# Optimization experiments

Hardware: AMD Instinct MI355X
Metric: run time of the kernel (lower is better)

## Reference

```python
import jax, jax.numpy as jnp
import numpy as np

IN_DIM, OUT_DIM, NUM, K = 512, 512, 5, 3
BATCH = 4096


def extend_grid(grid, k):
    # grid: (in_dim, num+1) -> (in_dim, num+1+2k), uniform step extension on both sides
    h = (grid[:, -1:] - grid[:, :1]) / (grid.shape[1] - 1)
    left = grid[:, :1] - h * jnp.arange(k, 0, -1, dtype=grid.dtype)
    right = grid[:, -1:] + h * jnp.arange(1, k + 1, dtype=grid.dtype)
    return jnp.concatenate([left, grid, right], axis=1)


def b_batch(x, grid, k):
    # Cox-de Boor recursion. x: (in_dim, batch), grid: (in_dim, G) extended.
    xe = x[:, None, :]            # (in, 1, B)
    g = grid[:, :, None]          # (in, G, 1)
    B = ((xe >= g[:, :-1]) & (xe < g[:, 1:])).astype(x.dtype)  # degree-0 indicators
    for p in range(1, k + 1):     # unrolled over small fixed k
        left = (xe - g[:, : -(p + 1)]) / (g[:, p:-1] - g[:, : -(p + 1)])
        right = (g[:, p + 1:] - xe) / (g[:, p + 1:] - g[:, 1:-p])
        B = left * B[:, :-1] + right * B[:, 1:]
    return B                      # (in_dim, NUM+K, batch)


def kan_forward(x, grid, weight, bias):
    batch = x.shape[0]
    xt = x.T                                            # (in, B)
    sp = b_batch(xt, extend_grid(grid, K), K)           # (in, num+k, B)
    sp = jnp.transpose(sp, (2, 1, 0))                   # (B, num+k, in)
    sb = jax.nn.silu(x)[:, None, :]                     # (B, 1, in)  base_fun branch
    gs = jnp.concatenate([sp, sb], axis=1)              # (B, num+k+1, in)
    acts = (gs * x[:, None, :]).reshape(batch, -1)      # einsum 'ijk,ik->ijk' + flatten
    return acts @ weight.T + bias                       # (B, out_dim)


def setup_inputs() -> dict:
    key = jax.random.key(0)
    k1, k2, k3 = jax.random.split(key, 3)
    x = jax.random.uniform(k1, (BATCH, IN_DIM), jnp.float32, -1.0, 1.0)
    grid = jnp.tile(jnp.linspace(-1.0, 1.0, NUM + 1, dtype=jnp.float32)[None, :], (IN_DIM, 1))
    in_multi = IN_DIM * (NUM + K + 1)
    weight = jax.random.normal(k2, (OUT_DIM, in_multi), jnp.float32) / np.sqrt(in_multi).astype(np.float32)
    bias = jax.random.normal(k3, (OUT_DIM,), jnp.float32) * 0.01
    return {"x": x, "grid": grid, "weight": weight, "bias": bias}


def reference(x, grid, weight, bias):
    return kan_forward(x, grid, weight, bias)
```

## Files before the change

kernel.cpp:

```cpp
#include <hip/hip_runtime.h>
#include <hip/hip_bf16.h>

#define IN_DIM  512
#define OUT_DIM 512
#define BATCH   4096
#define NBASIS  9
#define KDIM    (IN_DIM * NBASIS)

#define WOFF_WBF  0
#define WSZ_WBF   (OUT_DIM * KDIM * 2)
#define WOFF_ACTS (WOFF_WBF + WSZ_WBF)
#define WSZ_ACTS  (BATCH * KDIM * 2)
#define WOFF_PART (WOFF_ACTS + WSZ_ACTS)

typedef __attribute__((ext_vector_type(8))) short bf16x8;
typedef __attribute__((ext_vector_type(4))) float f32x4;
typedef __attribute__((ext_vector_type(8))) _Float16 h16x8;

#define NW_BLOCKS 2304

__global__ __launch_bounds__(256) void prep(const float4* __restrict__ w,
                                            short* __restrict__ wb,
                                            const float* __restrict__ x,
                                            const float* __restrict__ grid,
                                            __hip_bfloat16* __restrict__ acts) {
    int blk = blockIdx.x;
    if (blk < NW_BLOCKS) {
        int idx = blk * 256 + threadIdx.x;
        float4 v = w[idx];
        __hip_bfloat16 h[4] = {__float2bfloat16(v.x), __float2bfloat16(v.y),
                               __float2bfloat16(v.z), __float2bfloat16(v.w)};
        *reinterpret_cast<short4*>(wb + (size_t)idx * 4) = *reinterpret_cast<short4*>(h);
        return;
    }
    int idx = (blk - NW_BLOCKS) * 256 + threadIdx.x;
    int b = idx >> 9;
    int i = idx & 511;
    float xv = x[idx];
    float g0 = grid[i * 6];
    float g5 = grid[i * 6 + 5];
    float s = (xv - g0) * (5.0f / (g5 - g0));
    int mi = (int)s;
    mi = mi < 0 ? 0 : (mi > 4 ? 4 : mi);
    float u = s - (float)mi;
    float u2 = u * u, u3 = u2 * u;
    const float c6 = 1.0f / 6.0f;
    float om = 1.0f - u;
    float b0 = om * om * om * c6;
    float b1 = (3.0f * u3 - 6.0f * u2 + 4.0f) * c6;
    float b2 = (-3.0f * u3 + 3.0f * u2 + 3.0f * u + 1.0f) * c6;
    float b3 = u3 * c6;
    float sil = xv / (1.0f + __expf(-xv));

    __hip_bfloat16* dst = acts + (size_t)b * KDIM + i;
#pragma unroll
    for (int j = 0; j < 8; ++j) {
        int r = j - mi;
        float v = (r == 0) ? b0 : (r == 1) ? b1 : (r == 2) ? b2 : (r == 3) ? b3 : 0.0f;
        dst[j * IN_DIM] = __float2bfloat16(v * xv);
    }
    dst[8 * IN_DIM] = __float2bfloat16(sil * xv);
}

#define BM 128
#define BN 128
#define BK 64

__global__ __launch_bounds__(256) void gemm_kan(const short* __restrict__ A,
                                                const short* __restrict__ W,
                                                _Float16* __restrict__ part,
                                                int ksplit) {
    __shared__ __align__(16) short As[BM * BK];
    __shared__ __align__(16) short Ws[BN * BK];

    int nper = gridDim.x >> 3;
    int bid  = (blockIdx.x & 7) * nper + (blockIdx.x >> 3);

    int sk = bid >> 7;
    int mn = bid & 127;
    int bm = mn >> 2;
    int bn = mn & 3;

    int tid  = threadIdx.x;
    int lane = tid & 63;
    int wid  = tid >> 6;
    int wr   = wid >> 1;
    int wc   = wid & 1;

    const short* Ab = A + (size_t)(bm * BM) * KDIM + (size_t)sk * ksplit;
    const short* Wb = W + (size_t)(bn * BN) * KDIM + (size_t)sk * ksplit;
    int kiters = ksplit >> 6;

    f32x4 acc[4][4];
#pragma unroll
    for (int m = 0; m < 4; ++m)
#pragma unroll
        for (int n = 0; n < 4; ++n) acc[m][n] = (f32x4){0.f, 0.f, 0.f, 0.f};

    int srow = lane >> 3;
    int scol = ((lane & 7) ^ srow) * 8;

    for (int kb = 0; kb < kiters; ++kb) {
        int k0 = kb * BK;
        __syncthreads();
#pragma unroll
        for (int i = 0; i < 4; ++i) {
            int r0 = i * 32 + wid * 8;
            __builtin_amdgcn_global_load_lds(
                (const __attribute__((address_space(1))) void*)(Ab + (size_t)(r0 + srow) * KDIM + k0 + scol),
                (__attribute__((address_space(3))) void*)(&As[r0 * 64]),
                16, 0, 0);
        }
#pragma unroll
        for (int i = 0; i < 4; ++i) {
            int r0 = i * 32 + wid * 8;
            __builtin_amdgcn_global_load_lds(
                (const __attribute__((address_space(1))) void*)(Wb + (size_t)(r0 + srow) * KDIM + k0 + scol),
                (__attribute__((address_space(3))) void*)(&Ws[r0 * 64]),
                16, 0, 0);
        }
        __syncthreads();

        int g = lane >> 4;
        int fr = lane & 15;
#pragma unroll
        for (int ks = 0; ks < 2; ++ks) {
            int kk8 = ks * 4 + g;
            bf16x8 af[4], wf[4];
#pragma unroll
            for (int m = 0; m < 4; ++m) {
                int row = wr * 64 + m * 16 + fr;
                int slot = kk8 ^ (row & 7);
                af[m] = *reinterpret_cast<const bf16x8*>(&As[row * 64 + slot * 8]);
            }
#pragma unroll
            for (int n = 0; n < 4; ++n) {
                int col = wc * 64 + n * 16 + fr;
                int slot = kk8 ^ (col & 7);
                wf[n] = *reinterpret_cast<const bf16x8*>(&Ws[col * 64 + slot * 8]);
            }
#pragma unroll
            for (int m = 0; m < 4; ++m)
#pragma unroll
                for (int n = 0; n < 4; ++n)
                    acc[m][n] = __builtin_amdgcn_mfma_f32_16x16x32_bf16(af[m], wf[n], acc[m][n], 0, 0, 0);
        }
    }

    _Float16* p = part + (size_t)sk * BATCH * OUT_DIM;
    int crow0 = bm * BM + wr * 64 + (lane >> 4) * 4;
    int ccol0 = bn * BN + wc * 64 + (lane & 15);
#pragma unroll
    for (int m = 0; m < 4; ++m)
#pragma unroll
        for (int n = 0; n < 4; ++n)
#pragma unroll
            for (int r = 0; r < 4; ++r)
                p[(size_t)(crow0 + m * 16 + r) * OUT_DIM + ccol0 + n * 16] =
                    (_Float16)acc[m][n][r];
}

__global__ __launch_bounds__(256) void reduce_out(const _Float16* __restrict__ part,
                                                  const float4* __restrict__ bias,
                                                  float4* __restrict__ out,
                                                  int nsplit) {
    int idx = blockIdx.x * 256 + threadIdx.x;
    const size_t stride = (size_t)BATCH * OUT_DIM;
    float4 b0 = bias[(idx & 63) * 2];
    float4 b1 = bias[(idx & 63) * 2 + 1];
    float a[8] = {b0.x, b0.y, b0.z, b0.w, b1.x, b1.y, b1.z, b1.w};
#pragma unroll 4
    for (int s = 0; s < nsplit; ++s) {
        h16x8 v = *reinterpret_cast<const h16x8*>(part + (size_t)s * stride + (size_t)idx * 8);
#pragma unroll
        for (int j = 0; j < 8; ++j) a[j] += (float)v[j];
    }
    out[idx * 2]     = (float4){a[0], a[1], a[2], a[3]};
    out[idx * 2 + 1] = (float4){a[4], a[5], a[6], a[7]};
}

extern "C" void kernel_launch(void* const* d_in, const int* in_sizes, int n_in,
                              void* d_out, int out_size, void* d_ws, size_t ws_size,
                              hipStream_t stream) {
    (void)in_sizes; (void)n_in; (void)out_size;
    const float* x      = (const float*)d_in[0];
    const float* grid   = (const float*)d_in[1];
    const float* weight = (const float*)d_in[2];
    const float* bias   = (const float*)d_in[3];

    char* ws = (char*)d_ws;
    short*          wbf  = (short*)(ws + WOFF_WBF);
    __hip_bfloat16* acts = (__hip_bfloat16*)(ws + WOFF_ACTS);
    _Float16*       part = (_Float16*)(ws + WOFF_PART);

    size_t need4 = (size_t)WOFF_PART + 4ull * BATCH * OUT_DIM * 2;
    int splitk = (ws_size >= need4) ? 4 : 2;
    int ksplit = KDIM / splitk;

    prep<<<NW_BLOCKS + (BATCH * IN_DIM) / 256, 256, 0, stream>>>(
        (const float4*)weight, wbf, x, grid, acts);
    gemm_kan<<<128 * splitk, 256, 0, stream>>>((const short*)acts, wbf, part, ksplit);
    reduce_out<<<(BATCH * OUT_DIM / 8) / 256, 256, 0, stream>>>(
        part, (const float4*)bias, (float4*)d_out, splitk);
}
```

Before: 47.85 us.

## Fuse B-spline activation generation into GEMM A-tile loading with permuted weights

Activations are no longer materialised in global memory. Each GEMM block computes the cubic B-spline and SiLU terms for its A tile directly into shared memory, and the weight matrix is reordered at cast time so each input's 8 spline basis columns are contiguous. A small per-input grid table is precomputed. This removes the write and read of a roughly 37 MB bf16 activation buffer. In exchange, spline arithmetic is recomputed redundantly in every N-tile block and split-K is now fixed at 4 regardless of workspace size.

```diff
diff --git a/kernel.cpp b/kernel.cpp
--- a/kernel.cpp
+++ b/kernel.cpp
@@ -5,77 +5,74 @@
 #define OUT_DIM 512
 #define BATCH   4096
 #define NBASIS  9
-#define KDIM    (IN_DIM * NBASIS)
+#define KDIM    4608
+#define SPLITK  4
+#define KSPLIT  1152
 
 #define WOFF_WBF  0
 #define WSZ_WBF   (OUT_DIM * KDIM * 2)
-#define WOFF_ACTS (WOFF_WBF + WSZ_WBF)
-#define WSZ_ACTS  (BATCH * KDIM * 2)
-#define WOFF_PART (WOFF_ACTS + WSZ_ACTS)
+#define WOFF_PART (WOFF_WBF + WSZ_WBF)
+#define WSZ_PART  (SPLITK * BATCH * OUT_DIM * 2)
+#define WOFF_TBL  (WOFF_PART + WSZ_PART)
 
 typedef __attribute__((ext_vector_type(8))) short bf16x8;
 typedef __attribute__((ext_vector_type(4))) float f32x4;
 typedef __attribute__((ext_vector_type(8))) _Float16 h16x8;
 
-#define NW_BLOCKS 2304
-
-__global__ __launch_bounds__(256) void prep(const float4* __restrict__ w,
-                                            short* __restrict__ wb,
-                                            const float* __restrict__ x,
-                                            const float* __restrict__ grid,
-                                            __hip_bfloat16* __restrict__ acts) {
+__device__ __forceinline__ unsigned long long pack4(float a, float b, float c, float d) {
+    __hip_bfloat16 ha = __float2bfloat16(a), hb = __float2bfloat16(b),
+                   hc = __float2bfloat16(c), hd = __float2bfloat16(d);
+    return  (unsigned long long)*reinterpret_cast<unsigned short*>(&ha)
+         | ((unsigned long long)*reinterpret_cast<unsigned short*>(&hb) << 16)
+         | ((unsigned long long)*reinterpret_cast<unsigned short*>(&hc) << 32)
+         | ((unsigned long long)*reinterpret_cast<unsigned short*>(&hd) << 48);
+}
+
+__device__ __forceinline__ float silux(float z) {
+    return z * z / (1.0f + __expf(-z));
+}
+
+__global__ __launch_bounds__(256) void cast_w_perm(const float* __restrict__ w,
+                                                   short* __restrict__ wp,
+                                                   const float* __restrict__ grid,
+                                                   float2* __restrict__ tbl) {
     int blk = blockIdx.x;
-    if (blk < NW_BLOCKS) {
-        int idx = blk * 256 + threadIdx.x;
-        float4 v = w[idx];
-        __hip_bfloat16 h[4] = {__float2bfloat16(v.x), __float2bfloat16(v.y),
-                               __float2bfloat16(v.z), __float2bfloat16(v.w)};
-        *reinterpret_cast<short4*>(wb + (size_t)idx * 4) = *reinterpret_cast<short4*>(h);
+    if (blk == 1024) {
+        for (int i = threadIdx.x; i < IN_DIM; i += 256) {
+            float g0 = grid[i * 6];
+            float g5 = grid[i * 6 + 5];
+            tbl[i] = make_float2(g0, 5.0f / (g5 - g0));
+        }
         return;
     }
-    int idx = (blk - NW_BLOCKS) * 256 + threadIdx.x;
-    int b = idx >> 9;
+    int idx = blk * 256 + threadIdx.x;
+    int o = idx >> 9;
     int i = idx & 511;
-    float xv = x[idx];
-    float g0 = grid[i * 6];
-    float g5 = grid[i * 6 + 5];
-    float s = (xv - g0) * (5.0f / (g5 - g0));
-    int mi = (int)s;
-    mi = mi < 0 ? 0 : (mi > 4 ? 4 : mi);
-    float u = s - (float)mi;
-    float u2 = u * u, u3 = u2 * u;
-    const float c6 = 1.0f / 6.0f;
-    float om = 1.0f - u;
-    float b0 = om * om * om * c6;
-    float b1 = (3.0f * u3 - 6.0f * u2 + 4.0f) * c6;
-    float b2 = (-3.0f * u3 + 3.0f * u2 + 3.0f * u + 1.0f) * c6;
-    float b3 = u3 * c6;
-    float sil = xv / (1.0f + __expf(-xv));
-
-    __hip_bfloat16* dst = acts + (size_t)b * KDIM + i;
+    const float* wo = w + (size_t)o * KDIM;
+    bf16x8 v;
 #pragma unroll
     for (int j = 0; j < 8; ++j) {
-        int r = j - mi;
-        float v = (r == 0) ? b0 : (r == 1) ? b1 : (r == 2) ? b2 : (r == 3) ? b3 : 0.0f;
-        dst[j * IN_DIM] = __float2bfloat16(v * xv);
-    }
-    dst[8 * IN_DIM] = __float2bfloat16(sil * xv);
+        __hip_bfloat16 h = __float2bfloat16(wo[j * 512 + i]);
+        v[j] = *reinterpret_cast<short*>(&h);
+    }
+    *reinterpret_cast<bf16x8*>(wp + (size_t)o * KDIM + i * 8) = v;
+    __hip_bfloat16 h8 = __float2bfloat16(wo[8 * 512 + i]);
+    wp[(size_t)o * KDIM + 4096 + i] = *reinterpret_cast<short*>(&h8);
 }
 
 #define BM 128
 #define BN 128
 #define BK 64
 
-__global__ __launch_bounds__(256) void gemm_kan(const short* __restrict__ A,
-                                                const short* __restrict__ W,
-                                                _Float16* __restrict__ part,
-                                                int ksplit) {
+__global__ __launch_bounds__(256) void gemm_fused(const float* __restrict__ x,
+                                                  const short* __restrict__ Wp,
+                                                  const float2* __restrict__ tbl,
+                                                  _Float16* __restrict__ part) {
     __shared__ __align__(16) short As[BM * BK];
     __shared__ __align__(16) short Ws[BN * BK];
 
     int nper = gridDim.x >> 3;
     int bid  = (blockIdx.x & 7) * nper + (blockIdx.x >> 3);
-
     int sk = bid >> 7;
     int mn = bid & 127;
     int bm = mn >> 2;
@@ -87,9 +84,7 @@
     int wr   = wid >> 1;
     int wc   = wid & 1;
 
-    const short* Ab = A + (size_t)(bm * BM) * KDIM + (size_t)sk * ksplit;
-    const short* Wb = W + (size_t)(bn * BN) * KDIM + (size_t)sk * ksplit;
-    int kiters = ksplit >> 6;
+    const short* Wb = Wp + (size_t)(bn * BN) * KDIM + sk * KSPLIT;
 
     f32x4 acc[4][4];
 #pragma unroll
@@ -100,28 +95,69 @@
     int srow = lane >> 3;
     int scol = ((lane & 7) ^ srow) * 8;
 
-    for (int kb = 0; kb < kiters; ++kb) {
-        int k0 = kb * BK;
+    int arow  = tid >> 1;
+    int sbase = (tid & 1) * 4;
+    int r7    = arow & 7;
+    const float* xrow = x + (size_t)(bm * BM + arow) * IN_DIM;
+
+    for (int kb = 0; kb < KSPLIT / BK; ++kb) {
+        int k0l = kb * BK;
+        int k0g = sk * KSPLIT + k0l;
         __syncthreads();
+
 #pragma unroll
         for (int i = 0; i < 4; ++i) {
             int r0 = i * 32 + wid * 8;
             __builtin_amdgcn_global_load_lds(
-                (const __attribute__((address_space(1))) void*)(Ab + (size_t)(r0 + srow) * KDIM + k0 + scol),
-                (__attribute__((address_space(3))) void*)(&As[r0 * 64]),
-                16, 0, 0);
-        }
-#pragma unroll
-        for (int i = 0; i < 4; ++i) {
-            int r0 = i * 32 + wid * 8;
-            __builtin_amdgcn_global_load_lds(
-                (const __attribute__((address_space(1))) void*)(Wb + (size_t)(r0 + srow) * KDIM + k0 + scol),
+                (const __attribute__((address_space(1))) void*)(Wb + (size_t)(r0 + srow) * KDIM + k0l + scol),
                 (__attribute__((address_space(3))) void*)(&Ws[r0 * 64]),
                 16, 0, 0);
         }
+
+        if (k0g < 4096) {
+            int i0 = k0g >> 3;
+#pragma unroll
+            for (int c = 0; c < 4; ++c) {
+                int s  = sbase + c;
+                int ii = i0 + (s ^ r7);
+                float xv = xrow[ii];
+                float2 t = tbl[ii];
+                float ss = (xv - t.x) * t.y;
+                int mi = (int)ss; mi = mi < 0 ? 0 : (mi > 4 ? 4 : mi);
+                float u  = ss - (float)mi;
+                float u2 = u * u, u3 = u2 * u;
+                float om = 1.0f - u;
+                float xb = xv * (1.0f / 6.0f);
+                float b0 = om * om * om * xb;
+                float b1 = (3.0f * u3 - 6.0f * u2 + 4.0f) * xb;
+                float b2 = (-3.0f * u3 + 3.0f * u2 + 3.0f * u + 1.0f) * xb;
+                float b3 = u3 * xb;
+                unsigned long long p = pack4(b0, b1, b2, b3);
+                unsigned sh = (unsigned)mi << 4;
+                unsigned long long l1 = p << (sh & 63);
+                unsigned long long r1 = p >> ((64u - sh) & 63);
+                unsigned long long lo = (sh == 64u) ? 0ull : l1;
+                unsigned long long hi = (sh == 0u) ? 0ull : ((sh == 64u) ? p : r1);
+                ulonglong2 v; v.x = lo; v.y = hi;
+                *reinterpret_cast<ulonglong2*>(&As[arow * 64 + s * 8]) = v;
+            }
+        } else {
+            int ib = k0g - 4096;
+#pragma unroll
+            for (int c = 0; c < 4; ++c) {
+                int s = sbase + c;
+                const float* xp = xrow + ib + (s ^ r7) * 8;
+                float4 xa = *reinterpret_cast<const float4*>(xp);
+                float4 xc = *reinterpret_cast<const float4*>(xp + 4);
+                ulonglong2 v;
+                v.x = pack4(silux(xa.x), silux(xa.y), silux(xa.z), silux(xa.w));
+                v.y = pack4(silux(xc.x), silux(xc.y), silux(xc.z), silux(xc.w));
+                *reinterpret_cast<ulonglong2*>(&As[arow * 64 + s * 8]) = v;
+            }
+        }
         __syncthreads();
 
-        int g = lane >> 4;
+        int g  = lane >> 4;
         int fr = lane & 15;
 #pragma unroll
         for (int ks = 0; ks < 2; ++ks) {
@@ -162,15 +198,14 @@
 
 __global__ __launch_bounds__(256) void reduce_out(const _Float16* __restrict__ part,
                                                   const float4* __restrict__ bias,
-                                                  float4* __restrict__ out,
-                                                  int nsplit) {
+                                                  float4* __restrict__ out) {
     int idx = blockIdx.x * 256 + threadIdx.x;
     const size_t stride = (size_t)BATCH * OUT_DIM;
     float4 b0 = bias[(idx & 63) * 2];
     float4 b1 = bias[(idx & 63) * 2 + 1];
     float a[8] = {b0.x, b0.y, b0.z, b0.w, b1.x, b1.y, b1.z, b1.w};
-#pragma unroll 4
-    for (int s = 0; s < nsplit; ++s) {
+#pragma unroll
+    for (int s = 0; s < SPLITK; ++s) {
         h16x8 v = *reinterpret_cast<const h16x8*>(part + (size_t)s * stride + (size_t)idx * 8);
 #pragma unroll
         for (int j = 0; j < 8; ++j) a[j] += (float)v[j];
@@ -182,24 +217,19 @@
 extern "C" void kernel_launch(void* const* d_in, const int* in_sizes, int n_in,
                               void* d_out, int out_size, void* d_ws, size_t ws_size,
                               hipStream_t stream) {
-    (void)in_sizes; (void)n_in; (void)out_size;
+    (void)in_sizes; (void)n_in; (void)out_size; (void)ws_size;
     const float* x      = (const float*)d_in[0];
     const float* grid   = (const float*)d_in[1];
     const float* weight = (const float*)d_in[2];
     const float* bias   = (const float*)d_in[3];
 
     char* ws = (char*)d_ws;
-    short*          wbf  = (short*)(ws + WOFF_WBF);
-    __hip_bfloat16* acts = (__hip_bfloat16*)(ws + WOFF_ACTS);
-    _Float16*       part = (_Float16*)(ws + WOFF_PART);
-
-    size_t need4 = (size_t)WOFF_PART + 4ull * BATCH * OUT_DIM * 2;
-    int splitk = (ws_size >= need4) ? 4 : 2;
-    int ksplit = KDIM / splitk;
-
-    prep<<<NW_BLOCKS + (BATCH * IN_DIM) / 256, 256, 0, stream>>>(
-        (const float4*)weight, wbf, x, grid, acts);
-    gemm_kan<<<128 * splitk, 256, 0, stream>>>((const short*)acts, wbf, part, ksplit);
+    short*    wbf  = (short*)(ws + WOFF_WBF);
+    _Float16* part = (_Float16*)(ws + WOFF_PART);
+    float2*   tbl  = (float2*)(ws + WOFF_TBL);
+
+    cast_w_perm<<<1025, 256, 0, stream>>>(weight, wbf, grid, tbl);
+    gemm_fused<<<128 * SPLITK, 256, 0, stream>>>(x, wbf, tbl, part);
     reduce_out<<<(BATCH * OUT_DIM / 8) / 256, 256, 0, stream>>>(
-        part, (const float4*)bias, (float4*)d_out, splitk);
-}
+        part, (const float4*)bias, (float4*)d_out);
+}
```

New measurement: 64.78 us. 35.4% more time.

## Double-buffer LDS tiles in split-K GEMM with async global-to-LDS prefetch

Applied to the files above, without the earlier changes.

Converts the GEMM main loop to double-buffered LDS. The next K-tile is issued via global_load_lds while the current tile is being computed, using manual s_waitcnt vmcnt and s_barrier sequencing to overlap memory latency with MFMA work. Split-K is hardcoded to 4 and the workspace size check is removed, which makes the launch parameters compile-time constants. LDS use per block doubles, which may reduce occupancy, and the hand-written wait counts depend on the exact number of outstanding loads.

```diff
diff --git a/kernel.cpp b/kernel.cpp
--- a/kernel.cpp
+++ b/kernel.cpp
@@ -6,12 +6,16 @@
 #define BATCH   4096
 #define NBASIS  9
 #define KDIM    (IN_DIM * NBASIS)
+#define SPLITK  4
+#define KSPLIT  1152
+#define NSTEPS  18
 
 #define WOFF_WBF  0
 #define WSZ_WBF   (OUT_DIM * KDIM * 2)
 #define WOFF_ACTS (WOFF_WBF + WSZ_WBF)
 #define WSZ_ACTS  (BATCH * KDIM * 2)
 #define WOFF_PART (WOFF_ACTS + WSZ_ACTS)
+#define WSZ_PART  (SPLITK * BATCH * OUT_DIM * 2)
 
 typedef __attribute__((ext_vector_type(8))) short bf16x8;
 typedef __attribute__((ext_vector_type(4))) float f32x4;
@@ -68,14 +72,11 @@
 
 __global__ __launch_bounds__(256) void gemm_kan(const short* __restrict__ A,
                                                 const short* __restrict__ W,
-                                                _Float16* __restrict__ part,
-                                                int ksplit) {
-    __shared__ __align__(16) short As[BM * BK];
-    __shared__ __align__(16) short Ws[BN * BK];
-
-    int nper = gridDim.x >> 3;
-    int bid  = (blockIdx.x & 7) * nper + (blockIdx.x >> 3);
-
+                                                _Float16* __restrict__ part) {
+    __shared__ __align__(16) short As[2][BM * BK];
+    __shared__ __align__(16) short Ws[2][BN * BK];
+
+    int bid = (blockIdx.x & 7) * 64 + (blockIdx.x >> 3);
     int sk = bid >> 7;
     int mn = bid & 127;
     int bm = mn >> 2;
@@ -87,9 +88,8 @@
     int wr   = wid >> 1;
     int wc   = wid & 1;
 
-    const short* Ab = A + (size_t)(bm * BM) * KDIM + (size_t)sk * ksplit;
-    const short* Wb = W + (size_t)(bn * BN) * KDIM + (size_t)sk * ksplit;
-    int kiters = ksplit >> 6;
+    const short* Ab = A + (size_t)(bm * BM) * KDIM + sk * KSPLIT;
+    const short* Wb = W + (size_t)(bn * BN) * KDIM + sk * KSPLIT;
 
     f32x4 acc[4][4];
 #pragma unroll
@@ -100,15 +100,14 @@
     int srow = lane >> 3;
     int scol = ((lane & 7) ^ srow) * 8;
 
-    for (int kb = 0; kb < kiters; ++kb) {
+    auto stage = [&](int kb, int buf) {
         int k0 = kb * BK;
-        __syncthreads();
 #pragma unroll
         for (int i = 0; i < 4; ++i) {
             int r0 = i * 32 + wid * 8;
             __builtin_amdgcn_global_load_lds(
                 (const __attribute__((address_space(1))) void*)(Ab + (size_t)(r0 + srow) * KDIM + k0 + scol),
-                (__attribute__((address_space(3))) void*)(&As[r0 * 64]),
+                (__attribute__((address_space(3))) void*)(&As[buf][r0 * 64]),
                 16, 0, 0);
         }
 #pragma unroll
@@ -116,13 +115,29 @@
             int r0 = i * 32 + wid * 8;
             __builtin_amdgcn_global_load_lds(
                 (const __attribute__((address_space(1))) void*)(Wb + (size_t)(r0 + srow) * KDIM + k0 + scol),
-                (__attribute__((address_space(3))) void*)(&Ws[r0 * 64]),
+                (__attribute__((address_space(3))) void*)(&Ws[buf][r0 * 64]),
                 16, 0, 0);
         }
-        __syncthreads();
-
-        int g = lane >> 4;
-        int fr = lane & 15;
+    };
+
+    stage(0, 0);
+
+    int g  = lane >> 4;
+    int fr = lane & 15;
+    for (int kb = 0; kb < NSTEPS; ++kb) {
+        int cur = kb & 1;
+        __builtin_amdgcn_sched_barrier(0);
+        asm volatile("s_barrier" ::: "memory");
+        if (kb + 1 < NSTEPS) {
+            stage(kb + 1, cur ^ 1);
+            asm volatile("s_waitcnt vmcnt(8)\n\ts_barrier" ::: "memory");
+        } else {
+            asm volatile("s_waitcnt vmcnt(0)\n\ts_barrier" ::: "memory");
+        }
+        __builtin_amdgcn_sched_barrier(0);
+
+        const short* Ac = &As[cur][0];
+        const short* Wc = &Ws[cur][0];
 #pragma unroll
         for (int ks = 0; ks < 2; ++ks) {
             int kk8 = ks * 4 + g;
@@ -131,13 +146,13 @@
             for (int m = 0; m < 4; ++m) {
                 int row = wr * 64 + m * 16 + fr;
                 int slot = kk8 ^ (row & 7);
-                af[m] = *reinterpret_cast<const bf16x8*>(&As[row * 64 + slot * 8]);
+                af[m] = *reinterpret_cast<const bf16x8*>(&Ac[row * 64 + slot * 8]);
             }
 #pragma unroll
             for (int n = 0; n < 4; ++n) {
                 int col = wc * 64 + n * 16 + fr;
                 int slot = kk8 ^ (col & 7);
-                wf[n] = *reinterpret_cast<const bf16x8*>(&Ws[col * 64 + slot * 8]);
+                wf[n] = *reinterpret_cast<const bf16x8*>(&Wc[col * 64 + slot * 8]);
             }
 #pragma unroll
             for (int m = 0; m < 4; ++m)
@@ -162,15 +177,14 @@
 
 __global__ __launch_bounds__(256) void reduce_out(const _Float16* __restrict__ part,
                                                   const float4* __restrict__ bias,
-                                                  float4* __restrict__ out,
-                                                  int nsplit) {
+                                                  float4* __restrict__ out) {
     int idx = blockIdx.x * 256 + threadIdx.x;
     const size_t stride = (size_t)BATCH * OUT_DIM;
     float4 b0 = bias[(idx & 63) * 2];
     float4 b1 = bias[(idx & 63) * 2 + 1];
     float a[8] = {b0.x, b0.y, b0.z, b0.w, b1.x, b1.y, b1.z, b1.w};
-#pragma unroll 4
-    for (int s = 0; s < nsplit; ++s) {
+#pragma unroll
+    for (int s = 0; s < SPLITK; ++s) {
         h16x8 v = *reinterpret_cast<const h16x8*>(part + (size_t)s * stride + (size_t)idx * 8);
 #pragma unroll
         for (int j = 0; j < 8; ++j) a[j] += (float)v[j];
@@ -182,7 +196,7 @@
 extern "C" void kernel_launch(void* const* d_in, const int* in_sizes, int n_in,
                               void* d_out, int out_size, void* d_ws, size_t ws_size,
                               hipStream_t stream) {
-    (void)in_sizes; (void)n_in; (void)out_size;
+    (void)in_sizes; (void)n_in; (void)out_size; (void)ws_size;
     const float* x      = (const float*)d_in[0];
     const float* grid   = (const float*)d_in[1];
     const float* weight = (const float*)d_in[2];
@@ -193,13 +207,9 @@
     __hip_bfloat16* acts = (__hip_bfloat16*)(ws + WOFF_ACTS);
     _Float16*       part = (_Float16*)(ws + WOFF_PART);
 
-    size_t need4 = (size_t)WOFF_PART + 4ull * BATCH * OUT_DIM * 2;
-    int splitk = (ws_size >= need4) ? 4 : 2;
-    int ksplit = KDIM / splitk;
-
     prep<<<NW_BLOCKS + (BATCH * IN_DIM) / 256, 256, 0, stream>>>(
         (const float4*)weight, wbf, x, grid, acts);
-    gemm_kan<<<128 * splitk, 256, 0, stream>>>((const short*)acts, wbf, part, ksplit);
+    gemm_kan<<<128 * SPLITK, 256, 0, stream>>>((const short*)acts, wbf, part);
     reduce_out<<<(BATCH * OUT_DIM / 8) / 256, 256, 0, stream>>>(
-        part, (const float4*)bias, (float4*)d_out, splitk);
-}
+        part, (const float4*)bias, (float4*)d_out);
+}
```

Result: no change. 47.93 us (+0.2%).
